# Optimization experiments

Hardware: AMD Instinct MI355X
Metric: run time of the kernel (lower is better)

The kernel has to match this reference:

```python
import jax, jax.numpy as jnp
import numpy as np

NUM_NODES = 10000


def setup_inputs() -> dict:
    key = jax.random.key(0)
    k1, k2, k3, k4 = jax.random.split(key, 4)
    x = jax.random.normal(k1, (NUM_NODES, 128), dtype=jnp.float32)
    edge_index = jax.random.randint(k2, (2, 640000), 0, NUM_NODES, dtype=jnp.int64)
    W = jax.random.normal(k3, (128, 128), dtype=jnp.float32) * (1.0 / np.sqrt(128))
    b = jax.random.normal(k4, (128,), dtype=jnp.float32) * 0.01
    return {"x": x, "edge_index": edge_index, "W": W, "b": b}


def reference(x, edge_index, W, b):
    src, dst = edge_index[0], edge_index[1]
    num_nodes = x.shape[0]
    # scatter-add: aggregated[dst] += x[src]
    aggregated = jax.ops.segment_sum(x[src], dst, num_segments=num_nodes)
    # in-degree normalization (clamped at 1)
    degree = jax.ops.segment_sum(jnp.ones_like(dst, dtype=x.dtype), dst,
                                 num_segments=num_nodes)
    degree = jnp.maximum(degree, 1.0)
    aggregated = aggregated / degree[:, None]
    # linear (y = h @ W.T + b) + ReLU
    out = jax.nn.relu(jnp.einsum('nd,od->no', aggregated + x, W) + b)
    return out
```

## Files before the change

kernel.cpp:

```cpp
#include <hip/hip_runtime.h>
#include <hip/hip_bf16.h>
#include <hip/hip_fp8.h>

#define NB    64
#define EPB   10000
#define NPAD  10240
#define NPT   40
#define NGEMM 625
#define LCAP  1024
#define SMEM_BYTES 40496

typedef __bf16 bf16_8 __attribute__((ext_vector_type(8)));
typedef float f32_2 __attribute__((ext_vector_type(2)));
typedef float f32_4 __attribute__((ext_vector_type(4)));
typedef float f32_8 __attribute__((ext_vector_type(8)));

__device__ __forceinline__ void gemm_role(unsigned char* smem, int bx,
    const float* __restrict__ x, const float* __restrict__ W,
    __hip_bfloat16* __restrict__ zb, unsigned char* __restrict__ zb8) {
  float* ctile = (float*)smem;
  const int rowbase = bx * 16;
  const int wid = threadIdx.x >> 6;
  const int lane = threadIdx.x & 63;
  const int m16 = lane & 15;
  const int quad = lane >> 4;

  union { bf16_8 v; __hip_bfloat16 h8[8]; } ac[4];
  const float* arow = x + (size_t)(rowbase + m16) * 128 + quad * 8;
#pragma unroll
  for (int kk = 0; kk < 4; ++kk) {
    f32_8 af = *(const f32_8*)(arow + kk * 32);
#pragma unroll
    for (int j = 0; j < 8; ++j) ac[kk].h8[j] = __float2bfloat16(af[j]);
  }
#pragma unroll
  for (int ct = 0; ct < 2; ++ct) {
    int colbase = wid * 32 + ct * 16;
    const float* brow = W + (size_t)(colbase + m16) * 128 + quad * 8;
    f32_4 c = {0.f, 0.f, 0.f, 0.f};
#pragma unroll
    for (int kk = 0; kk < 4; ++kk) {
      f32_8 bf = *(const f32_8*)(brow + kk * 32);
      union { bf16_8 v; __hip_bfloat16 h8[8]; } bc;
#pragma unroll
      for (int j = 0; j < 8; ++j) bc.h8[j] = __float2bfloat16(bf[j]);
      c = __builtin_amdgcn_mfma_f32_16x16x32_bf16(ac[kk].v, bc.v, c, 0, 0, 0);
    }
#pragma unroll
    for (int r = 0; r < 4; ++r)
      ctile[(quad * 4 + r) * 132 + colbase + m16] = c[r];
  }
  __syncthreads();

  const int row = threadIdx.x >> 4;
  const int cs = (threadIdx.x & 15) * 8;
  const float* src = ctile + row * 132 + cs;
  f32_4 a0 = *(const f32_4*)(src);
  f32_4 a1 = *(const f32_4*)(src + 4);
  union { uint4 u; __hip_bfloat16 h[8]; } hb;
  union { uint2 u; unsigned char c[8]; } q8;
#pragma unroll
  for (int j = 0; j < 4; ++j) {
    hb.h[j] = __float2bfloat16(a0[j]);
    hb.h[4 + j] = __float2bfloat16(a1[j]);
    q8.c[j] = __hip_fp8_e4m3(a0[j]).__x;
    q8.c[4 + j] = __hip_fp8_e4m3(a1[j]).__x;
  }
  *(uint4*)(zb + (size_t)(rowbase + row) * 128 + cs) = hb.u;
  *(uint2*)(zb8 + (size_t)(rowbase + row) * 128 + cs) = q8.u;
}

__device__ __forceinline__ void sort_role(unsigned char* smem, int b,
    const int* __restrict__ ei, int E,
    unsigned short* __restrict__ bins, unsigned int* __restrict__ combo) {
  int* h = (int*)smem;
  unsigned short* sorted = (unsigned short*)(smem + 20480);
  int* wsum = (int*)(smem + 40480);

  const int t = threadIdx.x;
  const int4* src4 = (const int4*)(ei) + b * (EPB / 4);
  const int4* dst4 = (const int4*)(ei + E) + b * (EPB / 4);

  for (int i = t; i < NPAD / 2; i += 256) h[i] = 0;
  __syncthreads();

#pragma unroll
  for (int k = 0; k < 4; ++k) {
    int i0 = t + k * 512;
    int4 d0 = dst4[i0];
    int4 d1 = dst4[i0 + 256];
    atomicAdd(&h[d0.x >> 1], 1 << ((d0.x & 1) * 16));
    atomicAdd(&h[d0.y >> 1], 1 << ((d0.y & 1) * 16));
    atomicAdd(&h[d0.z >> 1], 1 << ((d0.z & 1) * 16));
    atomicAdd(&h[d0.w >> 1], 1 << ((d0.w & 1) * 16));
    atomicAdd(&h[d1.x >> 1], 1 << ((d1.x & 1) * 16));
    atomicAdd(&h[d1.y >> 1], 1 << ((d1.y & 1) * 16));
    atomicAdd(&h[d1.z >> 1], 1 << ((d1.z & 1) * 16));
    atomicAdd(&h[d1.w >> 1], 1 << ((d1.w & 1) * 16));
  }
  {
    int4 d = dst4[2048 + t];
    atomicAdd(&h[d.x >> 1], 1 << ((d.x & 1) * 16));
    atomicAdd(&h[d.y >> 1], 1 << ((d.y & 1) * 16));
    atomicAdd(&h[d.z >> 1], 1 << ((d.z & 1) * 16));
    atomicAdd(&h[d.w >> 1], 1 << ((d.w & 1) * 16));
  }
  if (t < 196) {
    int4 d = dst4[2304 + t];
    atomicAdd(&h[d.x >> 1], 1 << ((d.x & 1) * 16));
    atomicAdd(&h[d.y >> 1], 1 << ((d.y & 1) * 16));
    atomicAdd(&h[d.z >> 1], 1 << ((d.z & 1) * 16));
    atomicAdd(&h[d.w >> 1], 1 << ((d.w & 1) * 16));
  }
  __syncthreads();

  int raw[NPT];
  const int lo = t * NPT;
  int sum = 0;
#pragma unroll
  for (int j = 0; j < NPT; j += 2) {
    int pair = h[(lo + j) >> 1];
    raw[j] = pair & 0xFFFF;
    raw[j + 1] = (pair >> 16) & 0xFFFF;
    sum += raw[j] + raw[j + 1];
  }
  int incl = sum;
#pragma unroll
  for (int off = 1; off < 64; off <<= 1) {
    int v = __shfl_up(incl, off);
    if ((t & 63) >= off) incl += v;
  }
  if ((t & 63) == 63) wsum[t >> 6] = incl;
  __syncthreads();
  int wb = 0;
  for (int w = 0; w < (t >> 6); ++w) wb += wsum[w];
  int run = wb + incl - sum;

  unsigned int cpack[NPT];
#pragma unroll
  for (int j = 0; j < NPT; j += 2) {
    int r0 = run; run += raw[j];
    int r1 = run; run += raw[j + 1];
    h[(lo + j) >> 1] = (r1 << 16) | r0;
    cpack[j]     = ((unsigned)raw[j] << 16) | (unsigned)r0;
    cpack[j + 1] = ((unsigned)raw[j + 1] << 16) | (unsigned)r1;
  }
  __syncthreads();

  unsigned int* crow = combo + (size_t)b * NPAD + lo;
#pragma unroll
  for (int j = 0; j < NPT; j += 4)
    *(uint4*)(crow + j) = make_uint4(cpack[j], cpack[j+1], cpack[j+2], cpack[j+3]);

#pragma unroll
  for (int k = 0; k < 4; ++k) {
    int i0 = t + k * 512;
    int4 s0 = src4[i0];
    int4 d0 = dst4[i0];
    int4 s1 = src4[i0 + 256];
    int4 d1 = dst4[i0 + 256];
    int ss[8] = {s0.x, s0.y, s0.z, s0.w, s1.x, s1.y, s1.z, s1.w};
    int dd[8] = {d0.x, d0.y, d0.z, d0.w, d1.x, d1.y, d1.z, d1.w};
#pragma unroll
    for (int u = 0; u < 8; ++u) {
      int nn = dd[u];
      int sh = (nn & 1) * 16;
      int pos = (atomicAdd(&h[nn >> 1], 1 << sh) >> sh) & 0xFFFF;
      sorted[pos] = (unsigned short)ss[u];
    }
  }
  {
    int4 s = src4[2048 + t];
    int4 d = dst4[2048 + t];
    int ss[4] = {s.x, s.y, s.z, s.w};
    int dd[4] = {d.x, d.y, d.z, d.w};
#pragma unroll
    for (int u = 0; u < 4; ++u) {
      int nn = dd[u];
      int sh = (nn & 1) * 16;
      int pos = (atomicAdd(&h[nn >> 1], 1 << sh) >> sh) & 0xFFFF;
      sorted[pos] = (unsigned short)ss[u];
    }
  }
  if (t < 196) {
    int4 s = src4[2304 + t];
    int4 d = dst4[2304 + t];
    int ss[4] = {s.x, s.y, s.z, s.w};
    int dd[4] = {d.x, d.y, d.z, d.w};
#pragma unroll
    for (int u = 0; u < 4; ++u) {
      int nn = dd[u];
      int sh = (nn & 1) * 16;
      int pos = (atomicAdd(&h[nn >> 1], 1 << sh) >> sh) & 0xFFFF;
      sorted[pos] = (unsigned short)ss[u];
    }
  }
  __syncthreads();

  unsigned int* outb = (unsigned int*)(bins + (size_t)b * EPB);
  const unsigned int* s32 = (const unsigned int*)sorted;
  for (int i = t; i < EPB / 2; i += 256) outb[i] = s32[i];
}

__global__ void __launch_bounds__(256) k_phase1(
    const float* __restrict__ x, const int* __restrict__ ei,
    const float* __restrict__ W,
    __hip_bfloat16* __restrict__ zb, unsigned char* __restrict__ zb8,
    unsigned short* __restrict__ bins, unsigned int* __restrict__ combo, int E) {
  __shared__ __align__(16) unsigned char smem[SMEM_BYTES];
  if (blockIdx.x < NB) sort_role(smem, blockIdx.x, ei, E, bins, combo);
  else gemm_role(smem, blockIdx.x - NB, x, W, zb, zb8);
}

__global__ void __launch_bounds__(256) k_agg(
    const unsigned int* __restrict__ combo, const unsigned short* __restrict__ bins,
    const unsigned char* __restrict__ zb8, const __hip_bfloat16* __restrict__ zb,
    const float* __restrict__ bias, float* __restrict__ out, int N) {
  __shared__ unsigned int trans[4][64];
  __shared__ unsigned short list[4][LCAP];

  const int t = threadIdx.x;
  const int wid = t >> 6;
  const int lane = t & 63;
  const int n0 = blockIdx.x * 4;

  if (t < 64) {
    uint4 cm = *(const uint4*)(combo + (size_t)t * NPAD + n0);
    trans[0][t] = cm.x; trans[1][t] = cm.y; trans[2][t] = cm.z; trans[3][t] = cm.w;
  }
  __syncthreads();

  const int n = n0 + wid;
  unsigned int cc = trans[wid][lane];
  int c = (int)(cc >> 16);
  int o = (int)(cc & 0xFFFF);

  int incl = c;
#pragma unroll
  for (int off = 1; off < 64; off <<= 1) {
    int v = __shfl_up(incl, off);
    if (lane >= off) incl += v;
  }
  const int m = __shfl(incl, 63);
  int p = incl - c;

  {
    const unsigned short* bk = bins + (size_t)lane * EPB + o;
    unsigned short* L = list[wid];
    unsigned short s0 = 0, s1 = 0, s2 = 0;
    if (c > 0) s0 = bk[0];
    if (c > 1) s1 = bk[1];
    if (c > 2) s2 = bk[2];
    if (c > 0 && p < LCAP) L[p] = s0;
    if (c > 1 && p + 1 < LCAP) L[p + 1] = s1;
    if (c > 2 && p + 2 < LCAP) L[p + 2] = s2;
    for (int j = 3; j < c; ++j)
      if (p + j < LCAP) L[p + j] = bk[j];
  }

  const int g = lane >> 4;
  const int sub = lane & 15;
  int mm = m < LCAP ? m : LCAP;
  const unsigned short* L = list[wid];
  const unsigned char* z8base = zb8 + sub * 8;

  float acc[8] = {0.f, 0.f, 0.f, 0.f, 0.f, 0.f, 0.f, 0.f};
  for (int e = 0; e < mm; e += 32) {
    uint2 v[8];
#pragma unroll
    for (int u = 0; u < 8; ++u) {
      int idx = e + u * 4 + g;
      v[u] = make_uint2(0u, 0u);
      if (idx < mm) {
        int s = L[idx];
        v[u] = *(const uint2*)(z8base + (size_t)s * 128);
      }
    }
#pragma unroll
    for (int u = 0; u < 8; ++u) {
      f32_2 p01 = __builtin_amdgcn_cvt_pk_f32_fp8((int)v[u].x, false);
      f32_2 p23 = __builtin_amdgcn_cvt_pk_f32_fp8((int)v[u].x, true);
      f32_2 p45 = __builtin_amdgcn_cvt_pk_f32_fp8((int)v[u].y, false);
      f32_2 p67 = __builtin_amdgcn_cvt_pk_f32_fp8((int)v[u].y, true);
      acc[0] += p01[0]; acc[1] += p01[1];
      acc[2] += p23[0]; acc[3] += p23[1];
      acc[4] += p45[0]; acc[5] += p45[1];
      acc[6] += p67[0]; acc[7] += p67[1];
    }
  }
#pragma unroll
  for (int k = 0; k < 8; ++k) {
    acc[k] += __shfl_xor(acc[k], 16);
    acc[k] += __shfl_xor(acc[k], 32);
  }

  if (g == 0 && n < N) {
    float inv = 1.f / (float)(m > 0 ? m : 1);
    bf16_8 zn = *(const bf16_8*)(zb + (size_t)n * 128 + sub * 8);
    f32_8 bv = *(const f32_8*)(bias + sub * 8);
    float r[8];
#pragma unroll
    for (int k = 0; k < 8; ++k) {
      float v2 = acc[k] * inv + (float)zn[k] + bv[k];
      r[k] = v2 > 0.f ? v2 : 0.f;
    }
    float* o2 = out + (size_t)n * 128 + sub * 8;
    *(float4*)(o2)     = make_float4(r[0], r[1], r[2], r[3]);
    *(float4*)(o2 + 4) = make_float4(r[4], r[5], r[6], r[7]);
  }
}

extern "C" void kernel_launch(void* const* d_in, const int* in_sizes, int n_in,
                              void* d_out, int out_size, void* d_ws, size_t ws_size,
                              hipStream_t stream) {
  const float* x = (const float*)d_in[0];
  const int* ei = (const int*)d_in[1];
  const float* W = (const float*)d_in[2];
  const float* b = (const float*)d_in[3];
  float* out = (float*)d_out;

  const int N = in_sizes[0] / 128;
  const int E = in_sizes[1] / 2;

  char* ws = (char*)d_ws;
  size_t off = 0;
  auto carve = [&](size_t bytes) {
    void* p = ws + off;
    off = (off + bytes + 255) & ~(size_t)255;
    return p;
  };
  __hip_bfloat16* zb = (__hip_bfloat16*)carve((size_t)N * 128 * 2);
  unsigned char* zb8 = (unsigned char*)carve((size_t)N * 128);
  unsigned short* bins = (unsigned short*)carve((size_t)NB * EPB * 2);
  unsigned int* combo = (unsigned int*)carve((size_t)NB * NPAD * 4);

  k_phase1<<<NB + NGEMM, 256, 0, stream>>>(x, ei, W, zb, zb8, bins, combo, E);
  k_agg<<<N / 4, 256, 0, stream>>>(combo, bins, zb8, zb, b, out, N);
}
```

Before: 96.22 us.

## Split edge sorting across 128 blocks and merge two bins per lane

```diff
diff --git a/kernel.cpp b/kernel.cpp
--- a/kernel.cpp
+++ b/kernel.cpp
@@ -2,13 +2,13 @@
 #include <hip/hip_bf16.h>
 #include <hip/hip_fp8.h>
 
-#define NB    64
-#define EPB   10000
+#define NB    128
+#define EPB   5000
 #define NPAD  10240
 #define NPT   40
 #define NGEMM 625
 #define LCAP  1024
-#define SMEM_BYTES 40496
+#define SMEM_BYTES 30496
 
 typedef __bf16 bf16_8 __attribute__((ext_vector_type(8)));
 typedef float f32_2 __attribute__((ext_vector_type(2)));
@@ -75,7 +75,7 @@
     unsigned short* __restrict__ bins, unsigned int* __restrict__ combo) {
   int* h = (int*)smem;
   unsigned short* sorted = (unsigned short*)(smem + 20480);
-  int* wsum = (int*)(smem + 40480);
+  int* wsum = (int*)(smem + 30480);
 
   const int t = threadIdx.x;
   const int4* src4 = (const int4*)(ei) + b * (EPB / 4);
@@ -85,7 +85,7 @@
   __syncthreads();
 
 #pragma unroll
-  for (int k = 0; k < 4; ++k) {
+  for (int k = 0; k < 2; ++k) {
     int i0 = t + k * 512;
     int4 d0 = dst4[i0];
     int4 d1 = dst4[i0 + 256];
@@ -98,15 +98,8 @@
     atomicAdd(&h[d1.z >> 1], 1 << ((d1.z & 1) * 16));
     atomicAdd(&h[d1.w >> 1], 1 << ((d1.w & 1) * 16));
   }
-  {
-    int4 d = dst4[2048 + t];
-    atomicAdd(&h[d.x >> 1], 1 << ((d.x & 1) * 16));
-    atomicAdd(&h[d.y >> 1], 1 << ((d.y & 1) * 16));
-    atomicAdd(&h[d.z >> 1], 1 << ((d.z & 1) * 16));
-    atomicAdd(&h[d.w >> 1], 1 << ((d.w & 1) * 16));
-  }
-  if (t < 196) {
-    int4 d = dst4[2304 + t];
+  if (t < 226) {
+    int4 d = dst4[1024 + t];
     atomicAdd(&h[d.x >> 1], 1 << ((d.x & 1) * 16));
     atomicAdd(&h[d.y >> 1], 1 << ((d.y & 1) * 16));
     atomicAdd(&h[d.z >> 1], 1 << ((d.z & 1) * 16));
@@ -153,7 +146,7 @@
     *(uint4*)(crow + j) = make_uint4(cpack[j], cpack[j+1], cpack[j+2], cpack[j+3]);
 
 #pragma unroll
-  for (int k = 0; k < 4; ++k) {
+  for (int k = 0; k < 2; ++k) {
     int i0 = t + k * 512;
     int4 s0 = src4[i0];
     int4 d0 = dst4[i0];
@@ -169,22 +162,9 @@
       sorted[pos] = (unsigned short)ss[u];
     }
   }
-  {
-    int4 s = src4[2048 + t];
-    int4 d = dst4[2048 + t];
-    int ss[4] = {s.x, s.y, s.z, s.w};
-    int dd[4] = {d.x, d.y, d.z, d.w};
-#pragma unroll
-    for (int u = 0; u < 4; ++u) {
-      int nn = dd[u];
-      int sh = (nn & 1) * 16;
-      int pos = (atomicAdd(&h[nn >> 1], 1 << sh) >> sh) & 0xFFFF;
-      sorted[pos] = (unsigned short)ss[u];
-    }
-  }
-  if (t < 196) {
-    int4 s = src4[2304 + t];
-    int4 d = dst4[2304 + t];
+  if (t < 226) {
+    int4 s = src4[1024 + t];
+    int4 d = dst4[1024 + t];
     int ss[4] = {s.x, s.y, s.z, s.w};
     int dd[4] = {d.x, d.y, d.z, d.w};
 #pragma unroll
@@ -216,7 +196,7 @@
     const unsigned int* __restrict__ combo, const unsigned short* __restrict__ bins,
     const unsigned char* __restrict__ zb8, const __hip_bfloat16* __restrict__ zb,
     const float* __restrict__ bias, float* __restrict__ out, int N) {
-  __shared__ unsigned int trans[4][64];
+  __shared__ unsigned int trans[4][128];
   __shared__ unsigned short list[4][LCAP];
 
   const int t = threadIdx.x;
@@ -224,16 +204,18 @@
   const int lane = t & 63;
   const int n0 = blockIdx.x * 4;
 
-  if (t < 64) {
+  if (t < 128) {
     uint4 cm = *(const uint4*)(combo + (size_t)t * NPAD + n0);
     trans[0][t] = cm.x; trans[1][t] = cm.y; trans[2][t] = cm.z; trans[3][t] = cm.w;
   }
   __syncthreads();
 
   const int n = n0 + wid;
-  unsigned int cc = trans[wid][lane];
-  int c = (int)(cc >> 16);
-  int o = (int)(cc & 0xFFFF);
+  unsigned int cc0 = trans[wid][lane];
+  unsigned int cc1 = trans[wid][lane + 64];
+  const int c0 = (int)(cc0 >> 16), o0 = (int)(cc0 & 0xFFFF);
+  const int c1 = (int)(cc1 >> 16), o1 = (int)(cc1 & 0xFFFF);
+  const int c = c0 + c1;
 
   int incl = c;
 #pragma unroll
@@ -242,20 +224,26 @@
     if (lane >= off) incl += v;
   }
   const int m = __shfl(incl, 63);
-  int p = incl - c;
+  const int p = incl - c;
 
   {
-    const unsigned short* bk = bins + (size_t)lane * EPB + o;
     unsigned short* L = list[wid];
-    unsigned short s0 = 0, s1 = 0, s2 = 0;
-    if (c > 0) s0 = bk[0];
-    if (c > 1) s1 = bk[1];
-    if (c > 2) s2 = bk[2];
-    if (c > 0 && p < LCAP) L[p] = s0;
-    if (c > 1 && p + 1 < LCAP) L[p + 1] = s1;
-    if (c > 2 && p + 2 < LCAP) L[p + 2] = s2;
-    for (int j = 3; j < c; ++j)
-      if (p + j < LCAP) L[p + j] = bk[j];
+    const unsigned short* bk0 = bins + (size_t)lane * EPB + o0;
+    const unsigned short* bk1 = bins + (size_t)(lane + 64) * EPB + o1;
+    unsigned short a0 = 0, a1 = 0, b0 = 0, b1 = 0;
+    if (c0 > 0) a0 = bk0[0];
+    if (c0 > 1) a1 = bk0[1];
+    if (c1 > 0) b0 = bk1[0];
+    if (c1 > 1) b1 = bk1[1];
+    if (c0 > 0 && p < LCAP) L[p] = a0;
+    if (c0 > 1 && p + 1 < LCAP) L[p + 1] = a1;
+    for (int j = 2; j < c0; ++j)
+      if (p + j < LCAP) L[p + j] = bk0[j];
+    const int q = p + c0;
+    if (c1 > 0 && q < LCAP) L[q] = b0;
+    if (c1 > 1 && q + 1 < LCAP) L[q + 1] = b1;
+    for (int j = 2; j < c1; ++j)
+      if (q + j < LCAP) L[q + j] = bk1[j];
   }
 
   const int g = lane >> 4;
```

Result: faster. 94.14 us (-2.2%).
